# Kernel tuning notes

Measured on AMD Instinct MI355X. Metric: run time of the kernel, lower is better.

The kernel has to match this reference:

```python
import jax, jax.numpy as jnp
import numpy as np

N_ITERS = 1000   # n_iters default
LR = 0.1         # SGD lr default (schedule_lr=False -> constant lr)
EPS = 1e-8       # eps in LogMagTargetFrequencyLoss


def setup_inputs() -> dict:
    key = jax.random.key(0)
    k1, k2 = jax.random.split(key)
    # random log-magnitude target in dB (scaled to plausible dB range)
    target_dB = jax.random.normal(k1, (512,), dtype=jnp.float32) * 6.0
    # matches torch.rand(1, 16, 6) init of self.coefs / self.sos
    sos_init = jax.random.uniform(k2, (1, 16, 6), dtype=jnp.float32)
    return {"target_dB": target_dB, "sos_init": sos_init}


def _log_mag_loss(sos, target):
    """LogMagTargetFrequencyLoss: MSE between 20*log10|H(e^jw)| of the SOS
    cascade and the target dB response. sos: (1,16,6); target: (1,N)."""
    n = target.shape[-1]
    w = jnp.linspace(0.0, jnp.pi, n)                      # frequency grid (N,)
    zm = jnp.exp(-1j * w.astype(jnp.complex64))            # z^-1 on unit circle
    powers = jnp.stack([jnp.ones_like(zm), zm, zm * zm])   # (3, N): [1, z^-1, z^-2]
    b = sos[..., :3].astype(jnp.complex64)                 # (1,16,3)
    a = sos[..., 3:].astype(jnp.complex64)                 # (1,16,3)
    num = jnp.einsum('bsc,cn->bsn', b, powers)             # (1,16,N)
    den = jnp.einsum('bsc,cn->bsn', a, powers)             # (1,16,N)
    h = jnp.prod(num / den, axis=1)                        # cascade product -> (1,N)
    mag = 20.0 * jnp.log10(jnp.abs(h) + EPS)
    return jnp.mean((mag - target) ** 2)


def reference(target_dB, sos_init):
    target = target_dB.reshape(1, -1)
    grad_fn = jax.grad(_log_mag_loss)

    def step(sos, _):
        g = grad_fn(sos, target)
        return sos - LR * g, None   # plain SGD, constant lr (schedule_lr=False)

    sos, _ = jax.lax.scan(step, sos_init, None, length=N_ITERS)
    # pole_zero=False: out_sos aliases self.sos, so the returned tensor is the
    # post-step (final optimized) coefficients.
    return sos
```

## Files before the change

kernel.cpp:

```cpp
#include <hip/hip_runtime.h>
#include <math.h>

#define NITER 1000
#define LRATE 0.1f

typedef unsigned int v2u __attribute__((ext_vector_type(2)));

__device__ __forceinline__ float rcpf(float x) { return __builtin_amdgcn_rcpf(x); }

__device__ __forceinline__ float readlane_f(float v, int l) {
    return __int_as_float(__builtin_amdgcn_readlane(__float_as_int(v), l));
}

template<int CTRL>
__device__ __forceinline__ float dpp_mov(float v) {
    return __int_as_float(__builtin_amdgcn_update_dpp(0, __float_as_int(v), CTRL, 0xF, 0xF, true));
}

__device__ __forceinline__ int lane_id() {
    return __builtin_amdgcn_mbcnt_hi(~0u, __builtin_amdgcn_mbcnt_lo(~0u, 0u));
}

__device__ __forceinline__ void swap16(float& x, float& y) {
#if __has_builtin(__builtin_amdgcn_permlane16_swap)
    v2u r = __builtin_amdgcn_permlane16_swap(__float_as_uint(x), __float_as_uint(y), false, false);
    x = __uint_as_float(r[0]);
    y = __uint_as_float(r[1]);
#else
    const bool up = lane_id() & 16;
    const float send = up ? x : y;
    const float recv = __shfl_xor(send, 16);
    x = up ? recv : x;
    y = up ? y : recv;
#endif
}

__device__ __forceinline__ void swap32(float& x, float& y) {
#if __has_builtin(__builtin_amdgcn_permlane32_swap)
    v2u r = __builtin_amdgcn_permlane32_swap(__float_as_uint(x), __float_as_uint(y), false, false);
    x = __uint_as_float(r[0]);
    y = __uint_as_float(r[1]);
#else
    const bool up = lane_id() & 32;
    const float send = up ? x : y;
    const float recv = __shfl_xor(send, 32);
    x = up ? recv : x;
    y = up ? y : recv;
#endif
}

__global__ __launch_bounds__(1024, 1)
void sgd_filter_design_kernel(const float* __restrict__ target,
                              const float* __restrict__ sos_init,
                              float* __restrict__ out)
{
    const int t = threadIdx.x;
    const int w = t >> 6;
    const int L = t & 63;

    __shared__ __align__(16) float wq[16][576];
    __shared__ __align__(16) float Kbuf[576];

    const float PI = 3.14159265358979323846f;
    float C1[8], C2[8];
    #pragma unroll
    for (int f = 0; f < 8; ++f) {
        const int n = 8 * L + f;
        const float wr = PI * (float)n / 511.0f;
        const float c1 = cosf(wr);
        C1[f] = c1;
        C2[f] = 2.0f * c1 * c1 - 1.0f;
    }

    float mKt = 0.0f;
    int kaddr = 0;
    if (t < 512) {
        mKt = -0.03392925639869154f * target[t];
        kaddr = 8 * (t >> 3) + 4 * (t >> 5) + (t & 7);
    }

    const int sw = 8 * L + 4 * (L >> 2);
    const int col = ((L & 16) >> 2) | ((L & 32) >> 4) | (L & 1);
    const bool up1 = L & 1;

    float v0 = 0.0f;
    if (col < 6) v0 = sos_init[6 * w + col];
    float B0f = readlane_f(v0, 0);
    float B1f = readlane_f(v0, 1);
    float B2f = readlane_f(v0, 32);
    float A0f = readlane_f(v0, 33);
    float A1f = readlane_f(v0, 16);
    float A2f = readlane_f(v0, 17);

    for (int it = 0; it < NITER; ++it) {
        #pragma unroll
        for (int f = 0; f < 8; ++f) {
            asm volatile("" : "+v"(C1[f]), "+v"(C2[f]));
        }
        asm volatile("" : "+v"(mKt));

        const float P0 = fmaf(B0f, B0f, fmaf(B1f, B1f, B2f * B2f));
        float P1 = B1f * (B0f + B2f); P1 += P1;
        float P2 = B0f * B2f;         P2 += P2;
        const float Q0 = fmaf(A0f, A0f, fmaf(A1f, A1f, A2f * A2f));
        float Q1 = A1f * (A0f + A2f); Q1 += Q1;
        float Q2 = A0f * A2f;         Q2 += Q2;

        float imn[8], imd[8], qs[8];
        #pragma unroll
        for (int f = 0; f < 8; ++f) {
            float mn = fmaf(P2, C2[f], fmaf(P1, C1[f], P0));
            float md = fmaf(Q2, C2[f], fmaf(Q1, C1[f], Q0));
            mn = fmaxf(mn, 1e-18f);
            md = fmaxf(md, 1e-18f);
            const float rr = rcpf(mn * md);
            imn[f] = rr * md;
            imd[f] = rr * mn;
            qs[f] = mn * imd[f];
        }
        {
            const float4 q0 = {qs[0], qs[1], qs[2], qs[3]};
            const float4 q1 = {qs[4], qs[5], qs[6], qs[7]};
            *reinterpret_cast<float4*>(&wq[w][sw])     = q0;
            *reinterpret_cast<float4*>(&wq[w][sw + 4]) = q1;
        }
        __syncthreads();

        if (t < 512) {
            float p[16];
            #pragma unroll
            for (int ww = 0; ww < 16; ++ww) p[ww] = wq[ww][kaddr];
            p[0] *= p[8];  p[1] *= p[9];  p[2] *= p[10]; p[3] *= p[11];
            p[4] *= p[12]; p[5] *= p[13]; p[6] *= p[14]; p[7] *= p[15];
            p[0] *= p[4];  p[1] *= p[5];  p[2] *= p[6];  p[3] *= p[7];
            p[0] *= p[2];  p[1] *= p[3];
            p[0] *= p[1];
            Kbuf[kaddr] = fmaf(__log2f(p[0]), 0.10213724040f, mKt);
        }
        __syncthreads();

        const float4 k0 = *reinterpret_cast<const float4*>(&Kbuf[sw]);
        const float4 k1 = *reinterpret_cast<const float4*>(&Kbuf[sw + 4]);
        const float Kf[8] = {k0.x, k0.y, k0.z, k0.w, k1.x, k1.y, k1.z, k1.w};

        float X0, X1, X2, X3, X4, X5;
        #pragma unroll
        for (int f = 0; f < 8; ++f) {
            const float E = Kf[f] * imn[f];
            const float F = Kf[f] * imd[f];
            if (f == 0) {
                X0 = E;            X3 = F;
                X1 = E * C1[f];    X4 = F * C1[f];
                X2 = E * C2[f];    X5 = F * C2[f];
            } else {
                X0 += E;                      X3 += F;
                X1 = fmaf(E, C1[f], X1);      X4 = fmaf(F, C1[f], X4);
                X2 = fmaf(E, C2[f], X2);      X5 = fmaf(F, C2[f], X5);
            }
        }
        const float g6[6] = {X0, X1, X2, X3, X4, X5};

        float r4v[4];
        #pragma unroll
        for (int i = 0; i < 4; ++i) {
            float x = g6[i];
            float y = (i + 4 < 6) ? g6[i + 4] : 0.0f;
            swap16(x, y);
            r4v[i] = x + y;
        }
        float r2v[2];
        #pragma unroll
        for (int i = 0; i < 2; ++i) {
            float x = r4v[i], y = r4v[i + 2];
            swap32(x, y);
            r2v[i] = x + y;
        }
        float r1v;
        {
            const float x = r2v[0], y = r2v[1];
            const float P = up1 ? y : x, Q = up1 ? x : y;
            r1v = P + dpp_mov<0xB1>(Q);
        }
        r1v += dpp_mov<0x4E>(r1v);
        r1v += dpp_mov<0x128>(r1v);
        r1v += __shfl_xor(r1v, 4);

        const float S0 = readlane_f(r1v, 0);
        const float S1v = readlane_f(r1v, 1);
        const float S2v = readlane_f(r1v, 32);
        const float T0 = readlane_f(r1v, 33);
        const float T1v = readlane_f(r1v, 16);
        const float T2v = readlane_f(r1v, 17);

        const float gb0 = fmaf(B0f, S0, fmaf(B1f, S1v, B2f * S2v));
        const float gb1 = fmaf(B0f + B2f, S1v, B1f * S0);
        const float gb2 = fmaf(B0f, S2v, fmaf(B1f, S1v, B2f * S0));
        const float ga0 = fmaf(A0f, T0, fmaf(A1f, T1v, A2f * T2v));
        const float ga1 = fmaf(A0f + A2f, T1v, A1f * T0);
        const float ga2 = fmaf(A0f, T2v, fmaf(A1f, T1v, A2f * T0));

        B0f = fmaf(-LRATE, gb0, B0f);
        B1f = fmaf(-LRATE, gb1, B1f);
        B2f = fmaf(-LRATE, gb2, B2f);
        A0f = fmaf( LRATE, ga0, A0f);
        A1f = fmaf( LRATE, ga1, A1f);
        A2f = fmaf( LRATE, ga2, A2f);
    }

    if (L == 0) {
        out[6 * w + 0] = B0f;
        out[6 * w + 1] = B1f;
        out[6 * w + 2] = B2f;
        out[6 * w + 3] = A0f;
        out[6 * w + 4] = A1f;
        out[6 * w + 5] = A2f;
    }
}

extern "C" void kernel_launch(void* const* d_in, const int* in_sizes, int n_in,
                              void* d_out, int out_size, void* d_ws, size_t ws_size,
                              hipStream_t stream) {
    const float* target   = (const float*)d_in[0];
    const float* sos_init = (const float*)d_in[1];
    float* out = (float*)d_out;
    hipLaunchKernelGGL(sgd_filter_design_kernel, dim3(1), dim3(1024), 0, stream,
                       target, sos_init, out);
}
```

Baseline: 1.537 ms.

## Vectorize cascade product stage to float4 per thread and drop imd storage

The cross-wave product and log stage now uses 128 threads, each handling four frequencies with float4 LDS loads and a float4 store, in place of 512 threads doing scalar loads. The per-frequency imd array is removed: qs is computed directly and F is derived as E*qs, which cuts register pressure. The asm volatile register pins on C1/C2/mKt are also removed. The aim is fewer LDS instructions and a shorter critical path between the two barriers. The cost is a longer serial multiply chain per thread in two wavefronts, and small rounding differences from the altered F computation.

```diff
diff --git a/kernel.cpp b/kernel.cpp
--- a/kernel.cpp
+++ b/kernel.cpp
@@ -72,11 +72,15 @@
         C2[f] = 2.0f * c1 * c1 - 1.0f;
     }
 
-    float mKt = 0.0f;
-    int kaddr = 0;
-    if (t < 512) {
-        mKt = -0.03392925639869154f * target[t];
-        kaddr = 8 * (t >> 3) + 4 * (t >> 5) + (t & 7);
+    float4 mKt4 = {0.f, 0.f, 0.f, 0.f};
+    int kaddr4 = 0;
+    if (t < 128) {
+        const float4 tg = reinterpret_cast<const float4*>(target)[t];
+        mKt4.x = -0.03392925639869154f * tg.x;
+        mKt4.y = -0.03392925639869154f * tg.y;
+        mKt4.z = -0.03392925639869154f * tg.z;
+        mKt4.w = -0.03392925639869154f * tg.w;
+        kaddr4 = 4 * t + 4 * (t >> 3);
     }
 
     const int sw = 8 * L + 4 * (L >> 2);
@@ -93,12 +97,6 @@
     float A2f = readlane_f(v0, 17);
 
     for (int it = 0; it < NITER; ++it) {
-        #pragma unroll
-        for (int f = 0; f < 8; ++f) {
-            asm volatile("" : "+v"(C1[f]), "+v"(C2[f]));
-        }
-        asm volatile("" : "+v"(mKt));
-
         const float P0 = fmaf(B0f, B0f, fmaf(B1f, B1f, B2f * B2f));
         float P1 = B1f * (B0f + B2f); P1 += P1;
         float P2 = B0f * B2f;         P2 += P2;
@@ -106,7 +104,7 @@
         float Q1 = A1f * (A0f + A2f); Q1 += Q1;
         float Q2 = A0f * A2f;         Q2 += Q2;
 
-        float imn[8], imd[8], qs[8];
+        float imn[8], qs[8];
         #pragma unroll
         for (int f = 0; f < 8; ++f) {
             float mn = fmaf(P2, C2[f], fmaf(P1, C1[f], P0));
@@ -115,8 +113,7 @@
             md = fmaxf(md, 1e-18f);
             const float rr = rcpf(mn * md);
             imn[f] = rr * md;
-            imd[f] = rr * mn;
-            qs[f] = mn * imd[f];
+            qs[f] = (rr * mn) * mn;
         }
         {
             const float4 q0 = {qs[0], qs[1], qs[2], qs[3]};
@@ -126,16 +123,31 @@
         }
         __syncthreads();
 
-        if (t < 512) {
-            float p[16];
+        if (t < 128) {
+            float4 p0 = *reinterpret_cast<const float4*>(&wq[0][kaddr4]);
+            float4 p1 = *reinterpret_cast<const float4*>(&wq[1][kaddr4]);
+            float4 p2 = *reinterpret_cast<const float4*>(&wq[2][kaddr4]);
+            float4 p3 = *reinterpret_cast<const float4*>(&wq[3][kaddr4]);
             #pragma unroll
-            for (int ww = 0; ww < 16; ++ww) p[ww] = wq[ww][kaddr];
-            p[0] *= p[8];  p[1] *= p[9];  p[2] *= p[10]; p[3] *= p[11];
-            p[4] *= p[12]; p[5] *= p[13]; p[6] *= p[14]; p[7] *= p[15];
-            p[0] *= p[4];  p[1] *= p[5];  p[2] *= p[6];  p[3] *= p[7];
-            p[0] *= p[2];  p[1] *= p[3];
-            p[0] *= p[1];
-            Kbuf[kaddr] = fmaf(__log2f(p[0]), 0.10213724040f, mKt);
+            for (int ww = 4; ww < 16; ww += 4) {
+                const float4 u0 = *reinterpret_cast<const float4*>(&wq[ww + 0][kaddr4]);
+                const float4 u1 = *reinterpret_cast<const float4*>(&wq[ww + 1][kaddr4]);
+                const float4 u2 = *reinterpret_cast<const float4*>(&wq[ww + 2][kaddr4]);
+                const float4 u3 = *reinterpret_cast<const float4*>(&wq[ww + 3][kaddr4]);
+                p0.x *= u0.x; p0.y *= u0.y; p0.z *= u0.z; p0.w *= u0.w;
+                p1.x *= u1.x; p1.y *= u1.y; p1.z *= u1.z; p1.w *= u1.w;
+                p2.x *= u2.x; p2.y *= u2.y; p2.z *= u2.z; p2.w *= u2.w;
+                p3.x *= u3.x; p3.y *= u3.y; p3.z *= u3.z; p3.w *= u3.w;
+            }
+            p0.x *= p1.x; p0.y *= p1.y; p0.z *= p1.z; p0.w *= p1.w;
+            p2.x *= p3.x; p2.y *= p3.y; p2.z *= p3.z; p2.w *= p3.w;
+            p0.x *= p2.x; p0.y *= p2.y; p0.z *= p2.z; p0.w *= p2.w;
+            float4 Kv;
+            Kv.x = fmaf(__log2f(p0.x), 0.10213724040f, mKt4.x);
+            Kv.y = fmaf(__log2f(p0.y), 0.10213724040f, mKt4.y);
+            Kv.z = fmaf(__log2f(p0.z), 0.10213724040f, mKt4.z);
+            Kv.w = fmaf(__log2f(p0.w), 0.10213724040f, mKt4.w);
+            *reinterpret_cast<float4*>(&Kbuf[kaddr4]) = Kv;
         }
         __syncthreads();
 
@@ -147,7 +159,7 @@
         #pragma unroll
         for (int f = 0; f < 8; ++f) {
             const float E = Kf[f] * imn[f];
-            const float F = Kf[f] * imd[f];
+            const float F = E * qs[f];
             if (f == 0) {
                 X0 = E;            X3 = F;
                 X1 = E * C1[f];    X4 = F * C1[f];
```

Measured after the change: 1.860 ms. 1.21x slower.
